# Optimization experiments

Hardware: AMD Instinct MI355X
Metric: run time of the kernel (lower is better)

Reference implementation:

```python
import jax, jax.numpy as jnp
import numpy as np


def setup_inputs() -> dict:
    key = jax.random.key(0)
    ks = jax.random.split(key, 11)
    b, c, h, w = 16, 64, 16, 16
    F = 64  # num_filters
    O = 64  # num_outputs
    d_in = 2 * (c + 1)  # 130: concat of two (feature + coord) vectors
    s = 0.05
    return {
        "x_img": jax.random.normal(ks[0], (b, c, h, w), dtype=jnp.float32),
        "Wg0": jax.random.normal(ks[1], (F, d_in), dtype=jnp.float32) * s,
        "bg0": jax.random.normal(ks[2], (F,), dtype=jnp.float32) * s,
        "Wg1": jax.random.normal(ks[3], (F, F), dtype=jnp.float32) * s,
        "bg1": jax.random.normal(ks[4], (F,), dtype=jnp.float32) * s,
        "Wg2": jax.random.normal(ks[5], (F, F), dtype=jnp.float32) * s,
        "bg2": jax.random.normal(ks[6], (F,), dtype=jnp.float32) * s,
        "Wp": jax.random.normal(ks[7], (F, F), dtype=jnp.float32) * s,
        "bp": jax.random.normal(ks[8], (F,), dtype=jnp.float32) * s,
        "Wo": jax.random.normal(ks[9], (O, F), dtype=jnp.float32) * s,
        "bo": jax.random.normal(ks[10], (O,), dtype=jnp.float32) * s,
    }


def reference(x_img, Wg0, bg0, Wg1, bg1, Wg2, bg2, Wp, bp, Wo, bo):
    b, c, h, w = x_img.shape
    L = h * w
    # [b, L, c]: flatten spatial, move channels last
    feats = x_img.reshape(b, c, L).transpose(0, 2, 1)
    # append 1-d coordinate feature -> [b, L, c+1]
    coord = jnp.broadcast_to(
        jnp.arange(L, dtype=feats.dtype).reshape(1, L, 1), (b, L, 1)
    )
    feats = jnp.concatenate([feats, coord], axis=2)
    # pairwise broadcast-concat: pair[b, p, q] = [feats[b, q], feats[b, p]]
    d = feats.shape[-1]
    x_i = jnp.broadcast_to(feats[:, None, :, :], (b, L, L, d))
    x_j = jnp.broadcast_to(feats[:, :, None, :], (b, L, L, d))
    pair = jnp.concatenate([x_i, x_j], axis=3)  # [b, L, L, 2*(c+1)]
    # shared g-MLP (3 layers, ReLU)
    out = jax.nn.relu(jnp.einsum("bpqd,fd->bpqf", pair, Wg0) + bg0)
    out = jax.nn.relu(jnp.einsum("bpqf,gf->bpqg", out, Wg1) + bg1)
    out = jax.nn.relu(jnp.einsum("bpqf,gf->bpqg", out, Wg2) + bg2)
    # sum-reduce over both pair dims -> [b, F]
    out = out.sum(axis=(1, 2))
    # f-network
    out = jax.nn.relu(out @ Wp.T + bp)
    out = out @ Wo.T + bo
    return out
```

## Files before the change

kernel.cpp:

```cpp
#include <hip/hip_runtime.h>


typedef short s8v __attribute__((ext_vector_type(8)));
typedef short s4v __attribute__((ext_vector_type(4)));
typedef float f4v __attribute__((ext_vector_type(4)));

#define KEEP(x) asm volatile("" : "+v"(x))

#define MFMA16(a, b, c) __builtin_amdgcn_mfma_f32_16x16x16bf16_1k(a, b, c, 0, 0, 0)

__device__ __forceinline__ short bfr(float v) {
  return __builtin_bit_cast(short, (__bf16)v);
}
__device__ __forceinline__ f4v relu4(f4v v) {
  f4v z = {0.f, 0.f, 0.f, 0.f};
  return __builtin_elementwise_max(v, z);
}
__device__ __forceinline__ s8v cvt8(f4v a, f4v b) {
  s8v r;
  r[0] = bfr(a[0]); r[1] = bfr(a[1]); r[2] = bfr(a[2]); r[3] = bfr(a[3]);
  r[4] = bfr(b[0]); r[5] = bfr(b[1]); r[6] = bfr(b[2]); r[7] = bfr(b[3]);
  return r;
}
__device__ __forceinline__ s4v cvt4(f4v a) {
  s4v r;
  r[0] = bfr(a[0]); r[1] = bfr(a[1]); r[2] = bfr(a[2]); r[3] = bfr(a[3]);
  return r;
}
__device__ __forceinline__ f4v ldf4(const float* p) {
  return *(const f4v*)p;
}

__global__ __launch_bounds__(256) void k_pre(
    const float* __restrict__ x, const float* __restrict__ Wg0,
    const float* __restrict__ bg0, float* __restrict__ Ag,
    float* __restrict__ Bg) {
  __shared__ float ws[64 * 131];
  __shared__ float xs[64 * 17];

  const int t = threadIdx.x;
  const int b = blockIdx.x >> 4;
  const int l0 = (blockIdx.x & 15) * 16;

  for (int i = t; i < 64 * 130; i += 256) {
    int f = i / 130, d = i - f * 130;
    ws[f * 131 + d] = Wg0[i];
  }
  for (int i = t; i < 64 * 16; i += 256) {
    int ch = i >> 4, li = i & 15;
    xs[ch * 17 + li] = x[b * 16384 + ch * 256 + l0 + li];
  }
  __syncthreads();

  const int f = t & 63;
  const int w = t >> 6;
  float accA[4] = {0.f, 0.f, 0.f, 0.f};
  float accB[4] = {0.f, 0.f, 0.f, 0.f};
  for (int d = 0; d < 64; ++d) {
    float wa = ws[f * 131 + d];
    float wb = ws[f * 131 + 65 + d];
#pragma unroll
    for (int i = 0; i < 4; ++i) {
      float xv = xs[d * 17 + w + 4 * i];
      accA[i] += xv * wa;
      accB[i] += xv * wb;
    }
  }
  const float wca = ws[f * 131 + 64];
  const float wcb = ws[f * 131 + 129];
  const float bias = bg0[f];
#pragma unroll
  for (int i = 0; i < 4; ++i) {
    int l = l0 + w + 4 * i;
    Ag[(b * 256 + l) * 64 + f] = accA[i] + (float)l * wca;
    Bg[(b * 256 + l) * 64 + f] = accB[i] + (float)l * wcb + bias;
  }
}

__global__ __launch_bounds__(256, 2) void k_main(
    const float* __restrict__ Ag, const float* __restrict__ Bg,
    const float* __restrict__ Wg1, const float* __restrict__ bg1,
    const float* __restrict__ Wg2, const float* __restrict__ bg2,
    float* __restrict__ Part) {
  __shared__ __align__(16) float Bs[16 * 64];
  __shared__ float WaveS[4 * 64];

  const int t = threadIdx.x;
  const int wid = t >> 6;
  const int lane = t & 63;
  const int mm = lane & 15;
  const int quad = lane >> 4;
  const int b = blockIdx.y;
  const int blkx = blockIdx.x;
  const int qq = blkx & 3;
  const int p0 = (blkx >> 2) * 16;
  const int q0 = (qq * 4 + wid) * 16;

  {
    const f4v* Bb4 = (const f4v*)(Bg + (b * 256 + p0) * 64);
    ((f4v*)Bs)[t] = Bb4[t];
  }

  const float* Arow = Ag + (b * 256 + q0 + mm) * 64;
  f4v af0 = ldf4(Arow + quad * 8);
  f4v af1 = ldf4(Arow + quad * 8 + 4);
  f4v af2 = ldf4(Arow + 32 + quad * 8);
  f4v af3 = ldf4(Arow + 36 + quad * 8);

  s8v W1f[4][2];
  s4v W2f[4][4];
  f4v c1i[4], c2i[4];
#pragma unroll
  for (int gt = 0; gt < 4; ++gt) {
    c1i[gt] = ldf4(bg1 + gt * 16 + quad * 4);
    c2i[gt] = ldf4(bg2 + gt * 16 + quad * 4);
#pragma unroll
    for (int kh = 0; kh < 2; ++kh) {
      const float* r1 = Wg1 + (gt * 16 + mm) * 64 + kh * 32 + quad * 8;
      W1f[gt][kh] = cvt8(ldf4(r1), ldf4(r1 + 4));
    }
#pragma unroll
    for (int kt = 0; kt < 4; ++kt) {
      const float* r2 = Wg2 + (gt * 16 + mm) * 64 + kt * 16 + quad * 4;
      W2f[gt][kt] = cvt4(ldf4(r2));
    }
  }
#pragma unroll
  for (int gt = 0; gt < 4; ++gt) {
    KEEP(W1f[gt][0]); KEEP(W1f[gt][1]);
    KEEP(W2f[gt][0]); KEEP(W2f[gt][1]); KEEP(W2f[gt][2]); KEEP(W2f[gt][3]);
    KEEP(c1i[gt]); KEEP(c2i[gt]);
  }
  KEEP(af0); KEEP(af1); KEEP(af2); KEEP(af3);

  __syncthreads();

  f4v cs[4] = {{0.f,0.f,0.f,0.f},{0.f,0.f,0.f,0.f},
               {0.f,0.f,0.f,0.f},{0.f,0.f,0.f,0.f}};

  f4v bq0 = ldf4(Bs + quad * 8);
  f4v bq1 = ldf4(Bs + quad * 8 + 4);
  f4v bq2 = ldf4(Bs + 32 + quad * 8);
  f4v bq3 = ldf4(Bs + 36 + quad * 8);

  for (int ip = 0; ip < 16; ++ip) {
    const float* bn = Bs + ((ip < 15) ? ip + 1 : 15) * 64;
    f4v bn0 = ldf4(bn + quad * 8);
    f4v bn1 = ldf4(bn + quad * 8 + 4);
    f4v bn2 = ldf4(bn + 32 + quad * 8);
    f4v bn3 = ldf4(bn + 36 + quad * 8);

    s8v x0 = cvt8(relu4(af0 + bq0), relu4(af1 + bq1));
    s8v x1 = cvt8(relu4(af2 + bq2), relu4(af3 + bq3));

    s4v pk[4];
#pragma unroll
    for (int gt = 0; gt < 4; ++gt) {
      f4v a = c1i[gt];
      a = __builtin_amdgcn_mfma_f32_16x16x32_bf16(W1f[gt][0], x0, a, 0, 0, 0);
      a = __builtin_amdgcn_mfma_f32_16x16x32_bf16(W1f[gt][1], x1, a, 0, 0, 0);
      pk[gt] = cvt4(relu4(a));
    }
#pragma unroll
    for (int ot = 0; ot < 4; ++ot) {
      f4v a = c2i[ot];
      a = MFMA16(W2f[ot][0], pk[0], a);
      a = MFMA16(W2f[ot][1], pk[1], a);
      a = MFMA16(W2f[ot][2], pk[2], a);
      a = MFMA16(W2f[ot][3], pk[3], a);
      cs[ot] += relu4(a);
    }

    bq0 = bn0; bq1 = bn1; bq2 = bn2; bq3 = bn3;
  }

#pragma unroll
  for (int ot = 0; ot < 4; ++ot) {
#pragma unroll
    for (int r = 0; r < 4; ++r) {
      float v = cs[ot][r];
      v += __shfl_xor(v, 1);
      v += __shfl_xor(v, 2);
      v += __shfl_xor(v, 4);
      v += __shfl_xor(v, 8);
      if (mm == 0) WaveS[wid * 64 + ot * 16 + quad * 4 + r] = v;
    }
  }
  __syncthreads();
  if (t < 64) {
    float s = WaveS[t] + WaveS[64 + t] + WaveS[128 + t] + WaveS[192 + t];
    Part[(b * 64 + blkx) * 64 + t] = s;
  }
}

__global__ __launch_bounds__(256) void k_final(
    const float* __restrict__ Part, const float* __restrict__ Wp,
    const float* __restrict__ bp, const float* __restrict__ Wo,
    const float* __restrict__ bo, float* __restrict__ out) {
  __shared__ float red[4][64];
  __shared__ float sv[64], tv[64];
  const int b = blockIdx.x, t = threadIdx.x;
  const int o = t & 63, jw = t >> 6;
  const float* Pb = Part + b * 64 * 64;
  float s = 0.f;
#pragma unroll
  for (int j = 0; j < 16; ++j) s += Pb[(jw * 16 + j) * 64 + o];
  red[jw][o] = s;
  __syncthreads();
  if (t < 64) sv[t] = red[0][t] + red[1][t] + red[2][t] + red[3][t];
  __syncthreads();
  if (t < 64) {
    float acc = bp[t];
#pragma unroll
    for (int g4 = 0; g4 < 16; ++g4) {
      f4v wv = ldf4(Wp + t * 64 + g4 * 4);
      f4v xv = ldf4(sv + g4 * 4);
      acc += wv[0] * xv[0] + wv[1] * xv[1] + wv[2] * xv[2] + wv[3] * xv[3];
    }
    tv[t] = fmaxf(acc, 0.f);
  }
  __syncthreads();
  if (t < 64) {
    float o2 = bo[t];
#pragma unroll
    for (int g4 = 0; g4 < 16; ++g4) {
      f4v wv = ldf4(Wo + t * 64 + g4 * 4);
      f4v xv = ldf4(tv + g4 * 4);
      o2 += wv[0] * xv[0] + wv[1] * xv[1] + wv[2] * xv[2] + wv[3] * xv[3];
    }
    out[b * 64 + t] = o2;
  }
}

extern "C" void kernel_launch(void* const* d_in, const int* in_sizes, int n_in,
                              void* d_out, int out_size, void* d_ws, size_t ws_size,
                              hipStream_t stream) {
  const float* x   = (const float*)d_in[0];
  const float* Wg0 = (const float*)d_in[1];
  const float* bg0 = (const float*)d_in[2];
  const float* Wg1 = (const float*)d_in[3];
  const float* bg1 = (const float*)d_in[4];
  const float* Wg2 = (const float*)d_in[5];
  const float* bg2 = (const float*)d_in[6];
  const float* Wp  = (const float*)d_in[7];
  const float* bp  = (const float*)d_in[8];
  const float* Wo  = (const float*)d_in[9];
  const float* bo  = (const float*)d_in[10];
  float* out = (float*)d_out;

  float* Ag   = (float*)d_ws;
  float* Bg   = Ag + 16 * 256 * 64;
  float* Part = Bg + 16 * 256 * 64;

  k_pre<<<256, 256, 0, stream>>>(x, Wg0, bg0, Ag, Bg);
  k_main<<<dim3(64, 16), 256, 0, stream>>>(Ag, Bg, Wg1, bg1, Wg2, bg2, Part);
  k_final<<<16, 256, 0, stream>>>(Part, Wp, bp, Wo, bo, out);
}
```

Baseline: 116.2 us.

## Split main kernel into single-wave blocks and interleave independent MFMA chains

The main kernel now runs one wavefront per block (4096 blocks) instead of four. The shared-memory staging of B rows, the barriers and the cross-wave shared reduction are removed, so each wave reads B straight from global memory and writes its own partial sums. The MFMA sequences are reordered so the four output tiles issue independent accumulations back to back, which hides MFMA dependency latency. The final kernel reduces four times as many partials, and the B rows are re-read from global/L2 by each wave.

Result: slower. 131.3 us (+13.0%).

```diff
diff --git a/kernel.cpp b/kernel.cpp
--- a/kernel.cpp
+++ b/kernel.cpp
@@ -8,6 +8,7 @@
 #define KEEP(x) asm volatile("" : "+v"(x))
 
 #define MFMA16(a, b, c) __builtin_amdgcn_mfma_f32_16x16x16bf16_1k(a, b, c, 0, 0, 0)
+#define MFMA32(a, b, c) __builtin_amdgcn_mfma_f32_16x16x32_bf16(a, b, c, 0, 0, 0)
 
 __device__ __forceinline__ short bfr(float v) {
   return __builtin_bit_cast(short, (__bf16)v);
@@ -77,29 +78,18 @@
   }
 }
 
-__global__ __launch_bounds__(256, 2) void k_main(
+__global__ __launch_bounds__(64) void k_main(
     const float* __restrict__ Ag, const float* __restrict__ Bg,
     const float* __restrict__ Wg1, const float* __restrict__ bg1,
     const float* __restrict__ Wg2, const float* __restrict__ bg2,
     float* __restrict__ Part) {
-  __shared__ __align__(16) float Bs[16 * 64];
-  __shared__ float WaveS[4 * 64];
-
-  const int t = threadIdx.x;
-  const int wid = t >> 6;
-  const int lane = t & 63;
+  const int lane = threadIdx.x;
   const int mm = lane & 15;
   const int quad = lane >> 4;
   const int b = blockIdx.y;
-  const int blkx = blockIdx.x;
-  const int qq = blkx & 3;
-  const int p0 = (blkx >> 2) * 16;
-  const int q0 = (qq * 4 + wid) * 16;
-
-  {
-    const f4v* Bb4 = (const f4v*)(Bg + (b * 256 + p0) * 64);
-    ((f4v*)Bs)[t] = Bb4[t];
-  }
+  const int blk = blockIdx.x;
+  const int p0 = (blk >> 4) * 16;
+  const int q0 = (blk & 15) * 16;
 
   const float* Arow = Ag + (b * 256 + q0 + mm) * 64;
   f4v af0 = ldf4(Arow + quad * 8);
@@ -133,18 +123,17 @@
   }
   KEEP(af0); KEEP(af1); KEEP(af2); KEEP(af3);
 
-  __syncthreads();
-
   f4v cs[4] = {{0.f,0.f,0.f,0.f},{0.f,0.f,0.f,0.f},
                {0.f,0.f,0.f,0.f},{0.f,0.f,0.f,0.f}};
 
-  f4v bq0 = ldf4(Bs + quad * 8);
-  f4v bq1 = ldf4(Bs + quad * 8 + 4);
-  f4v bq2 = ldf4(Bs + 32 + quad * 8);
-  f4v bq3 = ldf4(Bs + 36 + quad * 8);
+  const float* Bbase = Bg + (b * 256 + p0) * 64;
+  f4v bq0 = ldf4(Bbase + quad * 8);
+  f4v bq1 = ldf4(Bbase + quad * 8 + 4);
+  f4v bq2 = ldf4(Bbase + 32 + quad * 8);
+  f4v bq3 = ldf4(Bbase + 36 + quad * 8);
 
   for (int ip = 0; ip < 16; ++ip) {
-    const float* bn = Bs + ((ip < 15) ? ip + 1 : 15) * 64;
+    const float* bn = Bbase + ((ip < 15) ? ip + 1 : 15) * 64;
     f4v bn0 = ldf4(bn + quad * 8);
     f4v bn1 = ldf4(bn + quad * 8 + 4);
     f4v bn2 = ldf4(bn + 32 + quad * 8);
@@ -153,23 +142,27 @@
     s8v x0 = cvt8(relu4(af0 + bq0), relu4(af1 + bq1));
     s8v x1 = cvt8(relu4(af2 + bq2), relu4(af3 + bq3));
 
+    f4v a1[4];
+#pragma unroll
+    for (int gt = 0; gt < 4; ++gt) a1[gt] = c1i[gt];
+#pragma unroll
+    for (int gt = 0; gt < 4; ++gt) a1[gt] = MFMA32(W1f[gt][0], x0, a1[gt]);
+#pragma unroll
+    for (int gt = 0; gt < 4; ++gt) a1[gt] = MFMA32(W1f[gt][1], x1, a1[gt]);
     s4v pk[4];
 #pragma unroll
-    for (int gt = 0; gt < 4; ++gt) {
-      f4v a = c1i[gt];
-      a = __builtin_amdgcn_mfma_f32_16x16x32_bf16(W1f[gt][0], x0, a, 0, 0, 0);
-      a = __builtin_amdgcn_mfma_f32_16x16x32_bf16(W1f[gt][1], x1, a, 0, 0, 0);
-      pk[gt] = cvt4(relu4(a));
-    }
-#pragma unroll
-    for (int ot = 0; ot < 4; ++ot) {
-      f4v a = c2i[ot];
-      a = MFMA16(W2f[ot][0], pk[0], a);
-      a = MFMA16(W2f[ot][1], pk[1], a);
-      a = MFMA16(W2f[ot][2], pk[2], a);
-      a = MFMA16(W2f[ot][3], pk[3], a);
-      cs[ot] += relu4(a);
-    }
+    for (int gt = 0; gt < 4; ++gt) pk[gt] = cvt4(relu4(a1[gt]));
+
+    f4v a2[4];
+#pragma unroll
+    for (int ot = 0; ot < 4; ++ot) a2[ot] = c2i[ot];
+#pragma unroll
+    for (int kt = 0; kt < 4; ++kt) {
+#pragma unroll
+      for (int ot = 0; ot < 4; ++ot) a2[ot] = MFMA16(W2f[ot][kt], pk[kt], a2[ot]);
+    }
+#pragma unroll
+    for (int ot = 0; ot < 4; ++ot) cs[ot] += relu4(a2[ot]);
 
     bq0 = bn0; bq1 = bn1; bq2 = bn2; bq3 = bn3;
   }
@@ -183,13 +176,9 @@
       v += __shfl_xor(v, 2);
       v += __shfl_xor(v, 4);
       v += __shfl_xor(v, 8);
-      if (mm == 0) WaveS[wid * 64 + ot * 16 + quad * 4 + r] = v;
-    }
-  }
-  __syncthreads();
-  if (t < 64) {
-    float s = WaveS[t] + WaveS[64 + t] + WaveS[128 + t] + WaveS[192 + t];
-    Part[(b * 64 + blkx) * 64 + t] = s;
+      if (mm == 0)
+        Part[(b * 256 + blk) * 64 + ot * 16 + quad * 4 + r] = v;
+    }
   }
 }
 
@@ -201,10 +190,10 @@
   __shared__ float sv[64], tv[64];
   const int b = blockIdx.x, t = threadIdx.x;
   const int o = t & 63, jw = t >> 6;
-  const float* Pb = Part + b * 64 * 64;
+  const float* Pb = Part + b * 256 * 64;
   float s = 0.f;
 #pragma unroll
-  for (int j = 0; j < 16; ++j) s += Pb[(jw * 16 + j) * 64 + o];
+  for (int j = 0; j < 64; ++j) s += Pb[(jw * 64 + j) * 64 + o];
   red[jw][o] = s;
   __syncthreads();
   if (t < 64) sv[t] = red[0][t] + red[1][t] + red[2][t] + red[3][t];
@@ -253,6 +242,6 @@
   float* Part = Bg + 16 * 256 * 64;
 
   k_pre<<<256, 256, 0, stream>>>(x, Wg0, bg0, Ag, Bg);
-  k_main<<<dim3(64, 16), 256, 0, stream>>>(Ag, Bg, Wg1, bg1, Wg2, bg2, Part);
+  k_main<<<dim3(256, 16), 64, 0, stream>>>(Ag, Bg, Wg1, bg1, Wg2, bg2, Part);
   k_final<<<16, 256, 0, stream>>>(Part, Wp, bp, Wo, bo, out);
 }
```

## Process two p rows per iteration with interleaved independent MFMA chains, halve grid

Applied to the files above, without the earlier changes.

Each k_main block now covers 32 p rows instead of 16, and the grid is halved to 512 blocks. The inner loop handles two p rows per iteration with two independent MFMA dependency chains, interleaved to hide MFMA latency. The software prefetch of B rows is replaced by direct LDS loads, and k_final is adjusted for half as many partials. In exchange, launch bounds drop to one block per SIMD set with more registers, and fewer blocks on a 256-CU part may lower occupancy.

After: 123.1 us. 5.9% more time.

```diff
diff --git a/kernel.cpp b/kernel.cpp
--- a/kernel.cpp
+++ b/kernel.cpp
@@ -8,6 +8,7 @@
 #define KEEP(x) asm volatile("" : "+v"(x))
 
 #define MFMA16(a, b, c) __builtin_amdgcn_mfma_f32_16x16x16bf16_1k(a, b, c, 0, 0, 0)
+#define MFMA32(a, b, c) __builtin_amdgcn_mfma_f32_16x16x32_bf16(a, b, c, 0, 0, 0)
 
 __device__ __forceinline__ short bfr(float v) {
   return __builtin_bit_cast(short, (__bf16)v);
@@ -77,12 +78,12 @@
   }
 }
 
-__global__ __launch_bounds__(256, 2) void k_main(
+__global__ __launch_bounds__(256, 1) void k_main(
     const float* __restrict__ Ag, const float* __restrict__ Bg,
     const float* __restrict__ Wg1, const float* __restrict__ bg1,
     const float* __restrict__ Wg2, const float* __restrict__ bg2,
     float* __restrict__ Part) {
-  __shared__ __align__(16) float Bs[16 * 64];
+  __shared__ __align__(16) float Bs[32 * 64];
   __shared__ float WaveS[4 * 64];
 
   const int t = threadIdx.x;
@@ -93,12 +94,13 @@
   const int b = blockIdx.y;
   const int blkx = blockIdx.x;
   const int qq = blkx & 3;
-  const int p0 = (blkx >> 2) * 16;
+  const int p0 = (blkx >> 2) * 32;
   const int q0 = (qq * 4 + wid) * 16;
 
   {
     const f4v* Bb4 = (const f4v*)(Bg + (b * 256 + p0) * 64);
     ((f4v*)Bs)[t] = Bb4[t];
+    ((f4v*)Bs)[t + 256] = Bb4[t + 256];
   }
 
   const float* Arow = Ag + (b * 256 + q0 + mm) * 64;
@@ -138,40 +140,52 @@
   f4v cs[4] = {{0.f,0.f,0.f,0.f},{0.f,0.f,0.f,0.f},
                {0.f,0.f,0.f,0.f},{0.f,0.f,0.f,0.f}};
 
-  f4v bq0 = ldf4(Bs + quad * 8);
-  f4v bq1 = ldf4(Bs + quad * 8 + 4);
-  f4v bq2 = ldf4(Bs + 32 + quad * 8);
-  f4v bq3 = ldf4(Bs + 36 + quad * 8);
-
-  for (int ip = 0; ip < 16; ++ip) {
-    const float* bn = Bs + ((ip < 15) ? ip + 1 : 15) * 64;
-    f4v bn0 = ldf4(bn + quad * 8);
-    f4v bn1 = ldf4(bn + quad * 8 + 4);
-    f4v bn2 = ldf4(bn + 32 + quad * 8);
-    f4v bn3 = ldf4(bn + 36 + quad * 8);
-
-    s8v x0 = cvt8(relu4(af0 + bq0), relu4(af1 + bq1));
-    s8v x1 = cvt8(relu4(af2 + bq2), relu4(af3 + bq3));
-
-    s4v pk[4];
-#pragma unroll
-    for (int gt = 0; gt < 4; ++gt) {
-      f4v a = c1i[gt];
-      a = __builtin_amdgcn_mfma_f32_16x16x32_bf16(W1f[gt][0], x0, a, 0, 0, 0);
-      a = __builtin_amdgcn_mfma_f32_16x16x32_bf16(W1f[gt][1], x1, a, 0, 0, 0);
-      pk[gt] = cvt4(relu4(a));
-    }
+#pragma clang loop unroll(disable)
+  for (int ip = 0; ip < 32; ip += 2) {
+    const float* bA = Bs + ip * 64;
+    const float* bB = bA + 64;
+    s8v xA0, xA1, xB0, xB1;
+    {
+      f4v a0 = ldf4(bA + quad * 8);
+      f4v a1_ = ldf4(bA + quad * 8 + 4);
+      f4v a2_ = ldf4(bA + 32 + quad * 8);
+      f4v a3_ = ldf4(bA + 36 + quad * 8);
+      xA0 = cvt8(relu4(af0 + a0), relu4(af1 + a1_));
+      xA1 = cvt8(relu4(af2 + a2_), relu4(af3 + a3_));
+      f4v b0 = ldf4(bB + quad * 8);
+      f4v b1_ = ldf4(bB + quad * 8 + 4);
+      f4v b2_ = ldf4(bB + 32 + quad * 8);
+      f4v b3_ = ldf4(bB + 36 + quad * 8);
+      xB0 = cvt8(relu4(af0 + b0), relu4(af1 + b1_));
+      xB1 = cvt8(relu4(af2 + b2_), relu4(af3 + b3_));
+    }
+
+    f4v a1A[4], a1B[4];
+#pragma unroll
+    for (int gt = 0; gt < 4; ++gt)
+      a1A[gt] = MFMA32(W1f[gt][1], xA1, MFMA32(W1f[gt][0], xA0, c1i[gt]));
+#pragma unroll
+    for (int gt = 0; gt < 4; ++gt)
+      a1B[gt] = MFMA32(W1f[gt][1], xB1, MFMA32(W1f[gt][0], xB0, c1i[gt]));
+
+    s4v pkA[4], pkB[4];
+#pragma unroll
+    for (int gt = 0; gt < 4; ++gt) pkA[gt] = cvt4(relu4(a1A[gt]));
+#pragma unroll
+    for (int gt = 0; gt < 4; ++gt) pkB[gt] = cvt4(relu4(a1B[gt]));
+
 #pragma unroll
     for (int ot = 0; ot < 4; ++ot) {
-      f4v a = c2i[ot];
-      a = MFMA16(W2f[ot][0], pk[0], a);
-      a = MFMA16(W2f[ot][1], pk[1], a);
-      a = MFMA16(W2f[ot][2], pk[2], a);
-      a = MFMA16(W2f[ot][3], pk[3], a);
-      cs[ot] += relu4(a);
-    }
-
-    bq0 = bn0; bq1 = bn1; bq2 = bn2; bq3 = bn3;
+      f4v aA = MFMA16(W2f[ot][3], pkA[3],
+               MFMA16(W2f[ot][2], pkA[2],
+               MFMA16(W2f[ot][1], pkA[1],
+               MFMA16(W2f[ot][0], pkA[0], c2i[ot]))));
+      f4v aB = MFMA16(W2f[ot][3], pkB[3],
+               MFMA16(W2f[ot][2], pkB[2],
+               MFMA16(W2f[ot][1], pkB[1],
+               MFMA16(W2f[ot][0], pkB[0], c2i[ot]))));
+      cs[ot] += relu4(aA) + relu4(aB);
+    }
   }
 
 #pragma unroll
@@ -189,7 +203,7 @@
   __syncthreads();
   if (t < 64) {
     float s = WaveS[t] + WaveS[64 + t] + WaveS[128 + t] + WaveS[192 + t];
-    Part[(b * 64 + blkx) * 64 + t] = s;
+    Part[(b * 32 + blkx) * 64 + t] = s;
   }
 }
 
@@ -201,10 +215,10 @@
   __shared__ float sv[64], tv[64];
   const int b = blockIdx.x, t = threadIdx.x;
   const int o = t & 63, jw = t >> 6;
-  const float* Pb = Part + b * 64 * 64;
+  const float* Pb = Part + b * 32 * 64;
   float s = 0.f;
 #pragma unroll
-  for (int j = 0; j < 16; ++j) s += Pb[(jw * 16 + j) * 64 + o];
+  for (int j = 0; j < 8; ++j) s += Pb[(jw * 8 + j) * 64 + o];
   red[jw][o] = s;
   __syncthreads();
   if (t < 64) sv[t] = red[0][t] + red[1][t] + red[2][t] + red[3][t];
@@ -253,6 +267,6 @@
   float* Part = Bg + 16 * 256 * 64;
 
   k_pre<<<256, 256, 0, stream>>>(x, Wg0, bg0, Ag, Bg);
-  k_main<<<dim3(64, 16), 256, 0, stream>>>(Ag, Bg, Wg1, bg1, Wg2, bg2, Part);
+  k_main<<<dim3(32, 16), 256, 0, stream>>>(Ag, Bg, Wg1, bg1, Wg2, bg2, Part);
   k_final<<<16, 256, 0, stream>>>(Part, Wp, bp, Wo, bo, out);
 }
```
